# Kernel optimization log

Hardware: AMD Instinct MI355X
Metric: run time of the kernel (lower is better)

The kernel has to match this reference:

```python
import jax, jax.numpy as jnp
import numpy as np

B, N, I = 8, 1024, 64
E, H, D = 2, 2, 128   # edge types, heads per layer, hidden dim
O = 64                # num_outputs
IN1 = E * H * D       # layer-1 filter input dim (concat of layer-0 heads)


def setup_inputs() -> dict:
    key = jax.random.key(0)
    ks = jax.random.split(key, 20)
    s = lambda f: 1.0 / np.sqrt(f)
    inp = {
        "nodes": jax.random.normal(ks[0], (B, N, I), jnp.float32),
        "edges": jax.random.normal(ks[1], (B, N, N, E), jnp.float32) * 0.1,
        "Wemb": jax.random.normal(ks[2], (I, D), jnp.float32) * s(I),
        "bemb": jnp.zeros((D,), jnp.float32),
        # layer 0 params: filter W, att nets a1/a2 (weight + bias), state bias
        "W0":   jax.random.normal(ks[3], (E, H, D, D), jnp.float32) * s(D),
        "A1w0": jax.random.normal(ks[4], (E, H, D), jnp.float32) * s(D),
        "A1b0": jnp.zeros((E, H), jnp.float32),
        "A2w0": jax.random.normal(ks[5], (E, H, D), jnp.float32) * s(D),
        "A2b0": jnp.zeros((E, H), jnp.float32),
        "SB0":  jnp.zeros((E, H, D), jnp.float32),
        # layer 1 params (input dim = E*H*D from concat)
        "W1":   jax.random.normal(ks[6], (E, H, IN1, D), jnp.float32) * s(IN1),
        "A1w1": jax.random.normal(ks[7], (E, H, D), jnp.float32) * s(D),
        "A1b1": jnp.zeros((E, H), jnp.float32),
        "A2w1": jax.random.normal(ks[8], (E, H, D), jnp.float32) * s(D),
        "A2b1": jnp.zeros((E, H), jnp.float32),
        "SB1":  jnp.zeros((E, H, D), jnp.float32),
        "Wout": jax.random.normal(ks[9], (D, O), jnp.float32) * s(D),
        "bout": jnp.zeros((O,), jnp.float32),
    }
    return inp


def _gat_layer(state, edges_ebnn, W, a1w, a1b, a2w, a2b, sb):
    # state: (B,N,Fin); W: (E,H,Fin,D); edges_ebnn: (E,1,B,N,N)
    Wh = jnp.einsum('bni,ehid->ehbnd', state, W)                    # (E,H,B,N,D)
    s1 = jnp.einsum('ehbnd,ehd->ehbn', Wh, a1w) + a1b[:, :, None, None]
    s2 = jnp.einsum('ehbnd,ehd->ehbn', Wh, a2w) + a2b[:, :, None, None]
    att = s1[..., :, None] + s2[..., None, :]                       # a1_i + a2_j
    att = jax.nn.leaky_relu(att, 0.2) + edges_ebnn                  # edge-type bias
    att = jax.nn.softmax(att, axis=-2)                              # torch dim=1 (over i)
    msg = jnp.einsum('ehbij,ehbjd->ehbid', att, Wh)                 # bmm aggregation
    return msg + sb[:, :, None, None, :]                            # (E,H,B,N,D)


def reference(nodes, edges, Wemb, bemb,
              W0, A1w0, A1b0, A2w0, A2b0, SB0,
              W1, A1w1, A1b1, A2w1, A2b1, SB1,
              Wout, bout):
    edges_e = jnp.transpose(edges, (3, 0, 1, 2))[:, None]           # (E,1,B,N,N)
    state = jax.nn.relu(nodes @ Wemb + bemb)                        # SlimFC embedding
    # layer 0: concat heads/edgetypes along feature dim (torch order jj outer, ii inner)
    m0 = _gat_layer(state, edges_e, W0, A1w0, A1b0, A2w0, A2b0, SB0)
    state = jnp.transpose(m0, (2, 3, 0, 1, 4)).reshape(B, N, E * H * D)
    # layer 1 (last): elu then mean over all heads/edgetypes
    m1 = jax.nn.elu(_gat_layer(state, edges_e, W1, A1w1, A1b1, A2w1, A2b1, SB1))
    state = jnp.mean(m1, axis=(0, 1))                               # (B,N,D)
    return state @ Wout + bout                                      # (B,N,O)
```

## Files before the change

kernel.cpp:

```cpp
#include <hip/hip_runtime.h>
#include <math.h>

#define NB 8
#define NN 1024
#define NI 64
#define EHC 4
#define ND 128
#define NO 64
#define FIN1 512
#define BN 8192
#define LOG2E 1.4426950408889634f

typedef __attribute__((ext_vector_type(8))) short short8;
typedef __attribute__((ext_vector_type(4))) float f32x4;
typedef __attribute__((ext_vector_type(2))) unsigned uint32x2;

__device__ __forceinline__ unsigned short f2bf(float f) {
    union { float f; unsigned u; } v; v.f = f;
    unsigned r = v.u + 0x7FFF + ((v.u >> 16) & 1);
    return (unsigned short)(r >> 16);
}
__device__ __forceinline__ unsigned short f2h(float f) {
    union { _Float16 h; unsigned short u; } v;
    v.h = (_Float16)f;
    return v.u;
}
__device__ __forceinline__ float h2f(unsigned short u) {
    union { unsigned short u; _Float16 h; } v;
    v.u = u;
    return (float)v.h;
}

__global__ void prepTk(const float* __restrict__ W0, const float* __restrict__ W1,
                       const float* __restrict__ Wemb, unsigned short* __restrict__ W0T,
                       unsigned short* __restrict__ W1T, unsigned short* __restrict__ WembT) {
    int idx = blockIdx.x * 256 + threadIdx.x;
    if (idx < EHC * ND * ND) {
        int eh = idx >> 14, d = (idx >> 7) & 127, k = idx & 127;
        W0T[idx] = f2bf(W0[((size_t)(eh * ND + k)) * ND + d]);
    }
    int idx1 = idx - EHC * ND * ND;
    if (idx1 >= 0 && idx1 < EHC * ND * FIN1) {
        int eh = idx1 >> 16;
        int r = idx1 & 65535;
        int d = r >> 9, k = r & 511;
        W1T[idx1] = f2bf(W1[((size_t)(eh * FIN1 + k)) * ND + d]);
    }
    int idx2 = idx - (EHC * ND * ND + EHC * ND * FIN1);
    if (idx2 >= 0 && idx2 < ND * NI) {
        int d = idx2 >> 6, k = idx2 & 63;
        WembT[idx2] = f2bf(Wemb[k * ND + d]);
    }
}

__global__ __launch_bounds__(256, 4) void embwh0k(
    const float* __restrict__ nodes, const unsigned short* __restrict__ WembT,
    const float* __restrict__ bemb, const unsigned short* __restrict__ W0T,
    unsigned short* __restrict__ WhT, const float* __restrict__ a1w,
    const float* __restrict__ a1b, const float* __restrict__ a2w,
    const float* __restrict__ a2b, float* __restrict__ s1, float* __restrict__ s2) {
    int id = blockIdx.x;
    int g = id & 7, s_ = id >> 3;
    int eh = s_ & 3;
    int row0 = ((s_ >> 2) * 8 + g) * 32;
    int t = threadIdx.x;
    int w = t >> 6, lane = t & 63;
    int m = lane & 15, quad = lane >> 4;

    __shared__ unsigned short stateL[32 * 136];

    f32x4 accE[2][2];
#pragma unroll
    for (int mt = 0; mt < 2; ++mt)
#pragma unroll
        for (int nt = 0; nt < 2; ++nt) accE[mt][nt] = (f32x4){0.f, 0.f, 0.f, 0.f};
#pragma unroll
    for (int kt = 0; kt < 2; ++kt) {
        short8 aE[2], bE[2];
#pragma unroll
        for (int mt = 0; mt < 2; ++mt) {
            const float* np = nodes + (size_t)(row0 + mt * 16 + m) * NI + kt * 32 + quad * 8;
            f32x4 v0 = *(const f32x4*)np;
            f32x4 v1 = *(const f32x4*)(np + 4);
            union { unsigned short us[8]; short8 s8; } pk;
#pragma unroll
            for (int r = 0; r < 4; ++r) {
                pk.us[r] = f2bf(v0[r]);
                pk.us[r + 4] = f2bf(v1[r]);
            }
            aE[mt] = pk.s8;
        }
#pragma unroll
        for (int nt = 0; nt < 2; ++nt)
            bE[nt] = *(const short8*)(WembT + (w * 32 + nt * 16 + m) * NI + kt * 32 + quad * 8);
#pragma unroll
        for (int mt = 0; mt < 2; ++mt)
#pragma unroll
            for (int nt = 0; nt < 2; ++nt)
                accE[mt][nt] =
                    __builtin_amdgcn_mfma_f32_16x16x32_bf16(aE[mt], bE[nt], accE[mt][nt], 0, 0, 0);
    }
#pragma unroll
    for (int mt = 0; mt < 2; ++mt)
#pragma unroll
        for (int nt = 0; nt < 2; ++nt) {
            int d = w * 32 + nt * 16 + m;
            float bb = bemb[d];
#pragma unroll
            for (int r = 0; r < 4; ++r) {
                float v = fmaxf(accE[mt][nt][r] + bb, 0.f);
                stateL[(mt * 16 + quad * 4 + r) * 136 + d] = f2bf(v);
            }
        }
    __syncthreads();

    f32x4 acc[2][2];
#pragma unroll
    for (int mt = 0; mt < 2; ++mt)
#pragma unroll
        for (int nt = 0; nt < 2; ++nt) acc[mt][nt] = (f32x4){0.f, 0.f, 0.f, 0.f};
#pragma unroll
    for (int k0 = 0; k0 < ND; k0 += 32) {
        short8 a[2], b[2];
#pragma unroll
        for (int mt = 0; mt < 2; ++mt)
            a[mt] = *(const short8*)&stateL[(mt * 16 + m) * 136 + k0 + quad * 8];
#pragma unroll
        for (int nt = 0; nt < 2; ++nt)
            b[nt] = *(const short8*)(W0T + ((size_t)(eh * ND + w * 32 + nt * 16 + m)) * ND +
                                     k0 + quad * 8);
#pragma unroll
        for (int mt = 0; mt < 2; ++mt)
#pragma unroll
            for (int nt = 0; nt < 2; ++nt)
                acc[mt][nt] =
                    __builtin_amdgcn_mfma_f32_16x16x32_bf16(a[mt], b[nt], acc[mt][nt], 0, 0, 0);
    }

    int b_ = row0 >> 10, i0b = row0 & 1023;
    int ehb = eh * NB + b_;
#pragma unroll
    for (int mt = 0; mt < 2; ++mt)
#pragma unroll
        for (int nt = 0; nt < 2; ++nt) {
            int d = w * 32 + nt * 16 + m;
            int i = i0b + mt * 16 + quad * 4;
            union { unsigned short us[4]; unsigned long long u64; } pk;
#pragma unroll
            for (int r = 0; r < 4; ++r) pk.us[r] = f2bf(acc[mt][nt][r]);
            *(unsigned long long*)(WhT + (((size_t)ehb) * ND + d) * NN + i) = pk.u64;
        }
    float w1a = a1w[eh * ND + w * 32 + m], w1b = a1w[eh * ND + w * 32 + 16 + m];
    float w2a = a2w[eh * ND + w * 32 + m], w2b = a2w[eh * ND + w * 32 + 16 + m];
    float p1[2][4], p2[2][4];
#pragma unroll
    for (int mt = 0; mt < 2; ++mt)
#pragma unroll
        for (int r = 0; r < 4; ++r) {
            p1[mt][r] = acc[mt][0][r] * w1a + acc[mt][1][r] * w1b;
            p2[mt][r] = acc[mt][0][r] * w2a + acc[mt][1][r] * w2b;
        }
#pragma unroll
    for (int off = 8; off >= 1; off >>= 1)
#pragma unroll
        for (int mt = 0; mt < 2; ++mt)
#pragma unroll
            for (int r = 0; r < 4; ++r) {
                p1[mt][r] += __shfl_xor(p1[mt][r], off);
                p2[mt][r] += __shfl_xor(p2[mt][r], off);
            }
    __shared__ float sred[2][4][4][8];
    if (m == 0) {
#pragma unroll
        for (int mt = 0; mt < 2; ++mt)
#pragma unroll
            for (int r = 0; r < 4; ++r) {
                sred[0][w][quad][mt * 4 + r] = p1[mt][r];
                sred[1][w][quad][mt * 4 + r] = p2[mt][r];
            }
    }
    __syncthreads();
    if (t < 32) {
        int mt = t >> 4, quad2 = (t >> 2) & 3, r = t & 3;
        int c = mt * 4 + r;
        float v = sred[0][0][quad2][c] + sred[0][1][quad2][c] + sred[0][2][quad2][c] +
                  sred[0][3][quad2][c];
        s1[(size_t)ehb * NN + i0b + t] = (v + a1b[eh]) * LOG2E;
    } else if (t < 64) {
        int tl = t - 32;
        int mt = tl >> 4, quad2 = (tl >> 2) & 3, r = tl & 3;
        int c = mt * 4 + r;
        float v = sred[1][0][quad2][c] + sred[1][1][quad2][c] + sred[1][2][quad2][c] +
                  sred[1][3][quad2][c];
        s2[(size_t)ehb * NN + i0b + tl] = (v + a2b[eh]) * LOG2E;
    }
}

__global__ __launch_bounds__(256, 4) void whgemm1k(
    const unsigned short* __restrict__ state, const unsigned short* __restrict__ WT,
    unsigned short* __restrict__ WhT, const float* __restrict__ a1w,
    const float* __restrict__ a1b, const float* __restrict__ a2w,
    const float* __restrict__ a2b, float* __restrict__ s1, float* __restrict__ s2) {
    int id = blockIdx.x;
    int g = id & 7, s_ = id >> 3;
    int eh = s_ & 3;
    int row0 = ((s_ >> 2) * 8 + g) * 32;
    int t = threadIdx.x;
    int w = t >> 6, lane = t & 63;
    int m = lane & 15, quad = lane >> 4;

    f32x4 acc[2][2];
#pragma unroll
    for (int mt = 0; mt < 2; ++mt)
#pragma unroll
        for (int nt = 0; nt < 2; ++nt) acc[mt][nt] = (f32x4){0.f, 0.f, 0.f, 0.f};

    const unsigned short* Ab = state + (size_t)(row0 + m) * FIN1 + quad * 8;
    const unsigned short* Bb = WT + ((size_t)eh * ND + w * 32 + m) * FIN1 + quad * 8;
#pragma unroll 4
    for (int k0 = 0; k0 < FIN1; k0 += 32) {
        short8 a[2], b[2];
#pragma unroll
        for (int mt = 0; mt < 2; ++mt)
            a[mt] = *(const short8*)(Ab + (size_t)mt * 16 * FIN1 + k0);
#pragma unroll
        for (int nt = 0; nt < 2; ++nt)
            b[nt] = *(const short8*)(Bb + (size_t)nt * 16 * FIN1 + k0);
#pragma unroll
        for (int mt = 0; mt < 2; ++mt)
#pragma unroll
            for (int nt = 0; nt < 2; ++nt)
                acc[mt][nt] =
                    __builtin_amdgcn_mfma_f32_16x16x32_bf16(a[mt], b[nt], acc[mt][nt], 0, 0, 0);
    }
    int b_ = row0 >> 10, i0b = row0 & 1023;
    int ehb = eh * NB + b_;
#pragma unroll
    for (int mt = 0; mt < 2; ++mt)
#pragma unroll
        for (int nt = 0; nt < 2; ++nt) {
            int d = w * 32 + nt * 16 + m;
            int i = i0b + mt * 16 + quad * 4;
            union { unsigned short us[4]; unsigned long long u64; } pk;
#pragma unroll
            for (int r = 0; r < 4; ++r) pk.us[r] = f2bf(acc[mt][nt][r]);
            *(unsigned long long*)(WhT + (((size_t)ehb) * ND + d) * NN + i) = pk.u64;
        }
    float w1a = a1w[eh * ND + w * 32 + m], w1b = a1w[eh * ND + w * 32 + 16 + m];
    float w2a = a2w[eh * ND + w * 32 + m], w2b = a2w[eh * ND + w * 32 + 16 + m];
    float p1[2][4], p2[2][4];
#pragma unroll
    for (int mt = 0; mt < 2; ++mt)
#pragma unroll
        for (int r = 0; r < 4; ++r) {
            p1[mt][r] = acc[mt][0][r] * w1a + acc[mt][1][r] * w1b;
            p2[mt][r] = acc[mt][0][r] * w2a + acc[mt][1][r] * w2b;
        }
#pragma unroll
    for (int off = 8; off >= 1; off >>= 1)
#pragma unroll
        for (int mt = 0; mt < 2; ++mt)
#pragma unroll
            for (int r = 0; r < 4; ++r) {
                p1[mt][r] += __shfl_xor(p1[mt][r], off);
                p2[mt][r] += __shfl_xor(p2[mt][r], off);
            }
    __shared__ float sred[2][4][4][8];
    if (m == 0) {
#pragma unroll
        for (int mt = 0; mt < 2; ++mt)
#pragma unroll
            for (int r = 0; r < 4; ++r) {
                sred[0][w][quad][mt * 4 + r] = p1[mt][r];
                sred[1][w][quad][mt * 4 + r] = p2[mt][r];
            }
    }
    __syncthreads();
    if (t < 32) {
        int mt = t >> 4, quad2 = (t >> 2) & 3, r = t & 3;
        int c = mt * 4 + r;
        float v = sred[0][0][quad2][c] + sred[0][1][quad2][c] + sred[0][2][quad2][c] +
                  sred[0][3][quad2][c];
        s1[(size_t)ehb * NN + i0b + t] = (v + a1b[eh]) * LOG2E;
    } else if (t < 64) {
        int tl = t - 32;
        int mt = tl >> 4, quad2 = (tl >> 2) & 3, r = tl & 3;
        int c = mt * 4 + r;
        float v = sred[1][0][quad2][c] + sred[1][1][quad2][c] + sred[1][2][quad2][c] +
                  sred[1][3][quad2][c];
        s2[(size_t)ehb * NN + i0b + tl] = (v + a2b[eh]) * LOG2E;
    }
}

template <int CONV>
__global__ __launch_bounds__(256, 4) void colsumk(const float* __restrict__ edges,
                                                  unsigned* __restrict__ edgesH,
                                                  const float* __restrict__ s1,
                                                  const float* __restrict__ s2,
                                                  float* __restrict__ Spart) {
    int jt = blockIdx.x, b = blockIdx.y, ic = blockIdx.z;
    int t = threadIdx.x;
    int jp = t & 31, is = t >> 5;
    int j = jt * 64 + jp * 2;
    __shared__ float s1L[4][128];
    for (int idx = t; idx < 512; idx += 256) {
        int eh = idx >> 7;
        s1L[eh][idx & 127] = s1[((size_t)eh * NB + b) * NN + ic * 128 + (idx & 127)];
    }
    __syncthreads();
    float s2v[4][2], acc4[4][2];
#pragma unroll
    for (int eh = 0; eh < 4; ++eh) {
        s2v[eh][0] = s2[((size_t)eh * NB + b) * NN + j];
        s2v[eh][1] = s2[((size_t)eh * NB + b) * NN + j + 1];
        acc4[eh][0] = 0.f;
        acc4[eh][1] = 0.f;
    }
    int irow0 = ic * 128 + is * 16;
    const float4* ep = (const float4*)edges + (size_t)(b * NN + irow0) * (NN / 2) + jt * 32 + jp;
    unsigned* ehw = edgesH + (size_t)(b * NN + irow0) * NN + j;
#pragma unroll 4
    for (int ii = 0; ii < 16; ++ii) {
        float e00, e10, e01, e11;
        if (CONV) {
            float4 ev = ep[(size_t)ii * (NN / 2)];
            unsigned p0 = (unsigned)f2h(ev.x * LOG2E) | ((unsigned)f2h(ev.y * LOG2E) << 16);
            unsigned p1 = (unsigned)f2h(ev.z * LOG2E) | ((unsigned)f2h(ev.w * LOG2E) << 16);
            *(uint32x2*)(ehw + (size_t)ii * NN) = (uint32x2){p0, p1};
            e00 = h2f((unsigned short)(p0 & 0xffff));
            e10 = h2f((unsigned short)(p0 >> 16));
            e01 = h2f((unsigned short)(p1 & 0xffff));
            e11 = h2f((unsigned short)(p1 >> 16));
        } else {
            uint32x2 pk = *(const uint32x2*)(ehw + (size_t)ii * NN);
            e00 = h2f((unsigned short)(pk.x & 0xffff));
            e10 = h2f((unsigned short)(pk.x >> 16));
            e01 = h2f((unsigned short)(pk.y & 0xffff));
            e11 = h2f((unsigned short)(pk.y >> 16));
        }
#pragma unroll
        for (int eh = 0; eh < 4; ++eh) {
            float sv = s1L[eh][is * 16 + ii];
            float x0 = sv + s2v[eh][0];
            x0 = fmaxf(x0, 0.2f * x0);
            acc4[eh][0] += __builtin_exp2f(x0 + (eh < 2 ? e00 : e10));
            float x1 = sv + s2v[eh][1];
            x1 = fmaxf(x1, 0.2f * x1);
            acc4[eh][1] += __builtin_exp2f(x1 + (eh < 2 ? e01 : e11));
        }
    }
    __shared__ float red[8][4][64];
#pragma unroll
    for (int eh = 0; eh < 4; ++eh) {
        red[is][eh][jp * 2] = acc4[eh][0];
        red[is][eh][jp * 2 + 1] = acc4[eh][1];
    }
    __syncthreads();
    if (t < 256) {
        int eho = t >> 6, jlo = t & 63;
        float Sv = 0.f;
#pragma unroll
        for (int isx = 0; isx < 8; ++isx) Sv += red[isx][eho][jlo];
        Spart[(((size_t)ic * EHC + eho) * NB + b) * NN + jt * 64 + jlo] = Sv;
    }
}

__global__ __launch_bounds__(512, 4) void msgk(const unsigned* __restrict__ edgesH,
                                               const unsigned short* __restrict__ WhT,
                                               const float* __restrict__ s1,
                                               const float* __restrict__ s2,
                                               const float* __restrict__ Spart,
                                               const float* __restrict__ sb,
                                               unsigned short* __restrict__ out0,
                                               float* __restrict__ out1, int mode) {
    int id = blockIdx.x;
    int b = id & 7;
    int s_ = id >> 3;
    int eh = s_ & 3;
    int itile = s_ >> 2;
    int e = eh >> 1;
    int i0 = itile * 64;
    int t = threadIdx.x;
    int w = t >> 6, lane = t & 63;
    int n = lane & 15, quad = lane >> 4;
    int jl = t & 63, ib = w;

    __shared__ float2 stL[NN];
    __shared__ unsigned short pA[2][64 * 72];

    int base = (eh * NB + b) * NN;
    const size_t pstr = (size_t)EHC * NB * NN;
    for (int jj = t; jj < NN; jj += 512) {
        float S = 0.f;
#pragma unroll
        for (int ic = 0; ic < 8; ++ic) S += Spart[(size_t)ic * pstr + base + jj];
        stL[jj] = make_float2(s2[base + jj], __builtin_log2f(S));
    }
    float s1r[8];
    {
        const f32x4* sp = (const f32x4*)(s1 + base + i0 + ib * 8);
        f32x4 v0 = sp[0], v1 = sp[1];
#pragma unroll
        for (int r = 0; r < 4; ++r) { s1r[r] = v0[r]; s1r[r + 4] = v1[r]; }
    }

    f32x4 acc[4];
#pragma unroll
    for (int nt = 0; nt < 4; ++nt) acc[nt] = (f32x4){0.f, 0.f, 0.f, 0.f};

    const unsigned short* Ab =
        WhT + ((size_t)base * ND + (size_t)(w * 16 + n) * NN) + quad * 8;
    const unsigned* ep = edgesH + (size_t)(b * NN + i0 + ib * 8) * NN + jl;
    __syncthreads();

    unsigned evA[8], evB[8];
    short8 aA[2], aB[2];

    auto loadE = [&](unsigned* ev, int j0) {
#pragma unroll
        for (int q = 0; q < 8; ++q) ev[q] = ep[(size_t)q * NN + j0];
    };
    auto loadA = [&](short8* av, int j0) {
#pragma unroll
        for (int kt = 0; kt < 2; ++kt)
            av[kt] = *(const short8*)(Ab + kt * 32 + j0);
    };
    auto pstep = [&](const unsigned* ev, const short8* av, int j0, int buf) {
        float2 stj = stL[j0 + jl];
#pragma unroll
        for (int q = 0; q < 8; ++q) {
            float edge = h2f((unsigned short)(e ? (ev[q] >> 16) : (ev[q] & 0xffff)));
            float x = s1r[q] + stj.x;
            x = fmaxf(x, 0.2f * x);
            pA[buf][(ib * 8 + q) * 72 + jl] = f2bf(__builtin_exp2f(x + edge - stj.y));
        }
        __syncthreads();
#pragma unroll
        for (int kt = 0; kt < 2; ++kt) {
            short8 bv[4];
#pragma unroll
            for (int nt = 0; nt < 4; ++nt)
                bv[nt] = *(const short8*)&pA[buf][(nt * 16 + n) * 72 + kt * 32 + quad * 8];
#pragma unroll
            for (int nt = 0; nt < 4; ++nt)
                acc[nt] =
                    __builtin_amdgcn_mfma_f32_16x16x32_bf16(av[kt], bv[nt], acc[nt], 0, 0, 0);
        }
    };

    loadE(evA, 0);
    loadA(aA, 0);
    for (int sp2 = 0; sp2 < 8; ++sp2) {
        int j0 = sp2 * 128;
        loadE(evB, j0 + 64);
        loadA(aB, j0 + 64);
        pstep(evA, aA, j0, 0);
        if (sp2 < 7) {
            loadE(evA, j0 + 128);
            loadA(aA, j0 + 128);
        }
        pstep(evB, aB, j0 + 64, 1);
    }

    {
        int d0 = w * 16 + quad * 4;
        f32x4 sbv = *(const f32x4*)&sb[eh * ND + d0];
#pragma unroll
        for (int nt = 0; nt < 4; ++nt) {
            int i = i0 + nt * 16 + n;
            if (mode == 0) {
                union { unsigned short us[4]; unsigned long long u64; } pk;
#pragma unroll
                for (int r = 0; r < 4; ++r) pk.us[r] = f2bf(acc[nt][r] + sbv[r]);
                *(unsigned long long*)(out0 + (size_t)(b * NN + i) * FIN1 + eh * ND + d0) =
                    pk.u64;
            } else {
                f32x4 vv;
#pragma unroll
                for (int r = 0; r < 4; ++r) {
                    float v = acc[nt][r] + sbv[r];
                    vv[r] = v > 0.f ? v : expm1f(v);
                }
                *(f32x4*)(out1 + ((size_t)(eh * NB + b) * NN + i) * ND + d0) = vv;
            }
        }
    }
}

__global__ __launch_bounds__(256) void finalk(const float* __restrict__ m1,
                                              const float* __restrict__ Wout,
                                              const float* __restrict__ bout,
                                              float* __restrict__ out) {
    int row0 = blockIdx.x * 16;
    int t = threadIdx.x;
    __shared__ float sF[16 * ND];
    __shared__ float wL[ND * NO];
    const size_t str = (size_t)BN * ND;
    for (int idx = t; idx < 16 * ND; idx += 256) {
        size_t r = (size_t)row0 * ND + idx;
        sF[idx] = 0.25f * (m1[r] + m1[r + str] + m1[r + 2 * str] + m1[r + 3 * str]);
    }
    for (int idx = t; idx < ND * NO; idx += 256) wL[idx] = Wout[idx];
    __syncthreads();
    int o = t & 63;
    int rr = t >> 6;
    float bo = bout[o];
#pragma unroll
    for (int q = 0; q < 4; ++q) {
        int r = rr * 4 + q;
        float acc = 0.f;
#pragma unroll 4
        for (int d = 0; d < ND; ++d) acc += sF[r * ND + d] * wL[d * NO + o];
        out[(size_t)(row0 + r) * NO + o] = acc + bo;
    }
}

extern "C" void kernel_launch(void* const* d_in, const int* in_sizes, int n_in,
                              void* d_out, int out_size, void* d_ws, size_t ws_size,
                              hipStream_t stream) {
    const float* nodes = (const float*)d_in[0];
    const float* edges = (const float*)d_in[1];
    const float* Wemb = (const float*)d_in[2];
    const float* bemb = (const float*)d_in[3];
    const float* W0 = (const float*)d_in[4];
    const float* A1w0 = (const float*)d_in[5];
    const float* A1b0 = (const float*)d_in[6];
    const float* A2w0 = (const float*)d_in[7];
    const float* A2b0 = (const float*)d_in[8];
    const float* SB0 = (const float*)d_in[9];
    const float* W1 = (const float*)d_in[10];
    const float* A1w1 = (const float*)d_in[11];
    const float* A1b1 = (const float*)d_in[12];
    const float* A2w1 = (const float*)d_in[13];
    const float* A2b1 = (const float*)d_in[14];
    const float* SB1 = (const float*)d_in[15];
    const float* Wout = (const float*)d_in[16];
    const float* bout = (const float*)d_in[17];
    float* out = (float*)d_out;

    char* p = (char*)d_ws;
    auto alloc = [&](size_t bytes) {
        char* r = p;
        p += (bytes + 255) & ~(size_t)255;
        return r;
    };
    unsigned short* W0T = (unsigned short*)alloc((size_t)EHC * ND * ND * 2);
    unsigned short* W1T = (unsigned short*)alloc((size_t)EHC * ND * FIN1 * 2);
    unsigned short* WembT = (unsigned short*)alloc((size_t)ND * NI * 2);
    unsigned short* WhT = (unsigned short*)alloc((size_t)EHC * BN * ND * 2);
    unsigned short* state1 = (unsigned short*)alloc((size_t)BN * FIN1 * 2);
    float* s1b = (float*)alloc((size_t)EHC * BN * 4);
    float* s2b = (float*)alloc((size_t)EHC * BN * 4);
    float* Spart = (float*)alloc((size_t)8 * EHC * BN * 4);
    float* m1 = (float*)alloc((size_t)EHC * BN * ND * 4);
    unsigned* edgesH = (unsigned*)alloc((size_t)NB * NN * NN * 4);

    prepTk<<<1312, 256, 0, stream>>>(W0, W1, Wemb, W0T, W1T, WembT);
    embwh0k<<<1024, 256, 0, stream>>>(nodes, WembT, bemb, W0T, WhT, A1w0, A1b0, A2w0, A2b0,
                                      s1b, s2b);
    colsumk<1><<<dim3(NN / 64, NB, 8), 256, 0, stream>>>(edges, edgesH, s1b, s2b, Spart);
    msgk<<<512, 512, 0, stream>>>(edgesH, WhT, s1b, s2b, Spart, SB0, state1, m1, 0);
    whgemm1k<<<1024, 256, 0, stream>>>(state1, W1T, WhT, A1w1, A1b1, A2w1, A2b1, s1b, s2b);
    colsumk<0><<<dim3(NN / 64, NB, 8), 256, 0, stream>>>(edges, edgesH, s1b, s2b, Spart);
    msgk<<<512, 512, 0, stream>>>(edgesH, WhT, s1b, s2b, Spart, SB1, state1, m1, 1);
    finalk<<<BN / 16, 256, 0, stream>>>(m1, Wout, bout, out);
}
```

Measured before the change: 267.4 us.

## Fuse ELU, head mean and output projection into msgk; halve i-tile

The final projection kernel is removed. The layer-1 message kernel now applies ELU, stages the result as bf16 in LDS, multiplies it by a transposed bf16 Wout with MFMA, and atomically accumulates a quarter of each head's contribution into the zeroed output buffer, which whgemm1k clears. The i-tile is halved to 32 rows so twice as many blocks launch, with a higher occupancy target. This drops the fp32 m1 round-trip through memory and one launch, but adds float atomics (order-dependent summation), bf16 rounding before the projection, and a doubled count of column-sum reloads per block.

```diff
diff --git a/kernel.cpp b/kernel.cpp
--- a/kernel.cpp
+++ b/kernel.cpp
@@ -32,8 +32,9 @@
 }
 
 __global__ void prepTk(const float* __restrict__ W0, const float* __restrict__ W1,
-                       const float* __restrict__ Wemb, unsigned short* __restrict__ W0T,
-                       unsigned short* __restrict__ W1T, unsigned short* __restrict__ WembT) {
+                       const float* __restrict__ Wemb, const float* __restrict__ Wout,
+                       unsigned short* __restrict__ W0T, unsigned short* __restrict__ W1T,
+                       unsigned short* __restrict__ WembT, unsigned short* __restrict__ WoutT) {
     int idx = blockIdx.x * 256 + threadIdx.x;
     if (idx < EHC * ND * ND) {
         int eh = idx >> 14, d = (idx >> 7) & 127, k = idx & 127;
@@ -50,6 +51,11 @@
     if (idx2 >= 0 && idx2 < ND * NI) {
         int d = idx2 >> 6, k = idx2 & 63;
         WembT[idx2] = f2bf(Wemb[k * ND + d]);
+    }
+    int idx3 = idx - (EHC * ND * ND + EHC * ND * FIN1 + ND * NI);
+    if (idx3 >= 0 && idx3 < ND * NO) {
+        int o = idx3 >> 7, d = idx3 & 127;
+        WoutT[idx3] = f2bf(Wout[d * NO + o]);
     }
 }
 
@@ -200,7 +206,8 @@
     const unsigned short* __restrict__ state, const unsigned short* __restrict__ WT,
     unsigned short* __restrict__ WhT, const float* __restrict__ a1w,
     const float* __restrict__ a1b, const float* __restrict__ a2w,
-    const float* __restrict__ a2b, float* __restrict__ s1, float* __restrict__ s2) {
+    const float* __restrict__ a2b, float* __restrict__ s1, float* __restrict__ s2,
+    float* __restrict__ outz) {
     int id = blockIdx.x;
     int g = id & 7, s_ = id >> 3;
     int eh = s_ & 3;
@@ -208,6 +215,11 @@
     int t = threadIdx.x;
     int w = t >> 6, lane = t & 63;
     int m = lane & 15, quad = lane >> 4;
+
+    {
+        f32x4 z = (f32x4){0.f, 0.f, 0.f, 0.f};
+        for (int idx = t; idx < 128; idx += 256) ((f32x4*)outz)[(size_t)id * 128 + idx] = z;
+    }
 
     f32x4 acc[2][2];
 #pragma unroll
@@ -365,28 +377,30 @@
     }
 }
 
-__global__ __launch_bounds__(512, 4) void msgk(const unsigned* __restrict__ edgesH,
+__global__ __launch_bounds__(512, 8) void msgk(const unsigned* __restrict__ edgesH,
                                                const unsigned short* __restrict__ WhT,
                                                const float* __restrict__ s1,
                                                const float* __restrict__ s2,
                                                const float* __restrict__ Spart,
                                                const float* __restrict__ sb,
                                                unsigned short* __restrict__ out0,
-                                               float* __restrict__ out1, int mode) {
+                                               const unsigned short* __restrict__ WoutT,
+                                               const float* __restrict__ bout,
+                                               float* __restrict__ out, int mode) {
     int id = blockIdx.x;
     int b = id & 7;
     int s_ = id >> 3;
     int eh = s_ & 3;
     int itile = s_ >> 2;
     int e = eh >> 1;
-    int i0 = itile * 64;
+    int i0 = itile * 32;
     int t = threadIdx.x;
     int w = t >> 6, lane = t & 63;
     int n = lane & 15, quad = lane >> 4;
     int jl = t & 63, ib = w;
 
     __shared__ float2 stL[NN];
-    __shared__ unsigned short pA[2][64 * 72];
+    __shared__ unsigned short pA[2][32 * 72];
 
     int base = (eh * NB + b) * NN;
     const size_t pstr = (size_t)EHC * NB * NN;
@@ -396,29 +410,28 @@
         for (int ic = 0; ic < 8; ++ic) S += Spart[(size_t)ic * pstr + base + jj];
         stL[jj] = make_float2(s2[base + jj], __builtin_log2f(S));
     }
-    float s1r[8];
+    float s1r[4];
     {
-        const f32x4* sp = (const f32x4*)(s1 + base + i0 + ib * 8);
-        f32x4 v0 = sp[0], v1 = sp[1];
-#pragma unroll
-        for (int r = 0; r < 4; ++r) { s1r[r] = v0[r]; s1r[r + 4] = v1[r]; }
-    }
-
-    f32x4 acc[4];
-#pragma unroll
-    for (int nt = 0; nt < 4; ++nt) acc[nt] = (f32x4){0.f, 0.f, 0.f, 0.f};
+        f32x4 v0 = *(const f32x4*)(s1 + base + i0 + ib * 4);
+#pragma unroll
+        for (int r = 0; r < 4; ++r) s1r[r] = v0[r];
+    }
+
+    f32x4 acc[2];
+#pragma unroll
+    for (int nt = 0; nt < 2; ++nt) acc[nt] = (f32x4){0.f, 0.f, 0.f, 0.f};
 
     const unsigned short* Ab =
         WhT + ((size_t)base * ND + (size_t)(w * 16 + n) * NN) + quad * 8;
-    const unsigned* ep = edgesH + (size_t)(b * NN + i0 + ib * 8) * NN + jl;
+    const unsigned* ep = edgesH + (size_t)(b * NN + i0 + ib * 4) * NN + jl;
     __syncthreads();
 
-    unsigned evA[8], evB[8];
+    unsigned evA[4], evB[4];
     short8 aA[2], aB[2];
 
     auto loadE = [&](unsigned* ev, int j0) {
 #pragma unroll
-        for (int q = 0; q < 8; ++q) ev[q] = ep[(size_t)q * NN + j0];
+        for (int q = 0; q < 4; ++q) ev[q] = ep[(size_t)q * NN + j0];
     };
     auto loadA = [&](short8* av, int j0) {
 #pragma unroll
@@ -428,21 +441,21 @@
     auto pstep = [&](const unsigned* ev, const short8* av, int j0, int buf) {
         float2 stj = stL[j0 + jl];
 #pragma unroll
-        for (int q = 0; q < 8; ++q) {
+        for (int q = 0; q < 4; ++q) {
             float edge = h2f((unsigned short)(e ? (ev[q] >> 16) : (ev[q] & 0xffff)));
             float x = s1r[q] + stj.x;
             x = fmaxf(x, 0.2f * x);
-            pA[buf][(ib * 8 + q) * 72 + jl] = f2bf(__builtin_exp2f(x + edge - stj.y));
+            pA[buf][(ib * 4 + q) * 72 + jl] = f2bf(__builtin_exp2f(x + edge - stj.y));
         }
         __syncthreads();
 #pragma unroll
         for (int kt = 0; kt < 2; ++kt) {
-            short8 bv[4];
-#pragma unroll
-            for (int nt = 0; nt < 4; ++nt)
+            short8 bv[2];
+#pragma unroll
+            for (int nt = 0; nt < 2; ++nt)
                 bv[nt] = *(const short8*)&pA[buf][(nt * 16 + n) * 72 + kt * 32 + quad * 8];
 #pragma unroll
-            for (int nt = 0; nt < 4; ++nt)
+            for (int nt = 0; nt < 2; ++nt)
                 acc[nt] =
                     __builtin_amdgcn_mfma_f32_16x16x32_bf16(av[kt], bv[nt], acc[nt], 0, 0, 0);
         }
@@ -462,56 +475,45 @@
         pstep(evB, aB, j0 + 64, 1);
     }
 
-    {
-        int d0 = w * 16 + quad * 4;
-        f32x4 sbv = *(const f32x4*)&sb[eh * ND + d0];
-#pragma unroll
-        for (int nt = 0; nt < 4; ++nt) {
+    int d0 = w * 16 + quad * 4;
+    f32x4 sbv = *(const f32x4*)&sb[eh * ND + d0];
+    if (mode == 0) {
+#pragma unroll
+        for (int nt = 0; nt < 2; ++nt) {
             int i = i0 + nt * 16 + n;
-            if (mode == 0) {
-                union { unsigned short us[4]; unsigned long long u64; } pk;
-#pragma unroll
-                for (int r = 0; r < 4; ++r) pk.us[r] = f2bf(acc[nt][r] + sbv[r]);
-                *(unsigned long long*)(out0 + (size_t)(b * NN + i) * FIN1 + eh * ND + d0) =
-                    pk.u64;
-            } else {
-                f32x4 vv;
-#pragma unroll
-                for (int r = 0; r < 4; ++r) {
-                    float v = acc[nt][r] + sbv[r];
-                    vv[r] = v > 0.f ? v : expm1f(v);
-                }
-                *(f32x4*)(out1 + ((size_t)(eh * NB + b) * NN + i) * ND + d0) = vv;
-            }
-        }
-    }
-}
-
-__global__ __launch_bounds__(256) void finalk(const float* __restrict__ m1,
-                                              const float* __restrict__ Wout,
-                                              const float* __restrict__ bout,
-                                              float* __restrict__ out) {
-    int row0 = blockIdx.x * 16;
-    int t = threadIdx.x;
-    __shared__ float sF[16 * ND];
-    __shared__ float wL[ND * NO];
-    const size_t str = (size_t)BN * ND;
-    for (int idx = t; idx < 16 * ND; idx += 256) {
-        size_t r = (size_t)row0 * ND + idx;
-        sF[idx] = 0.25f * (m1[r] + m1[r + str] + m1[r + 2 * str] + m1[r + 3 * str]);
-    }
-    for (int idx = t; idx < ND * NO; idx += 256) wL[idx] = Wout[idx];
-    __syncthreads();
-    int o = t & 63;
-    int rr = t >> 6;
-    float bo = bout[o];
-#pragma unroll
-    for (int q = 0; q < 4; ++q) {
-        int r = rr * 4 + q;
-        float acc = 0.f;
-#pragma unroll 4
-        for (int d = 0; d < ND; ++d) acc += sF[r * ND + d] * wL[d * NO + o];
-        out[(size_t)(row0 + r) * NO + o] = acc + bo;
+            union { unsigned short us[4]; unsigned long long u64; } pk;
+#pragma unroll
+            for (int r = 0; r < 4; ++r) pk.us[r] = f2bf(acc[nt][r] + sbv[r]);
+            *(unsigned long long*)(out0 + (size_t)(b * NN + i) * FIN1 + eh * ND + d0) = pk.u64;
+        }
+    } else {
+        __syncthreads();
+        unsigned short* eluL = (unsigned short*)pA;
+#pragma unroll
+        for (int nt = 0; nt < 2; ++nt) {
+            int il = nt * 16 + n;
+#pragma unroll
+            for (int r = 0; r < 4; ++r) {
+                float v = acc[nt][r] + sbv[r];
+                v = v > 0.f ? v : expm1f(v);
+                eluL[il * 136 + d0 + r] = f2bf(v);
+            }
+        }
+        __syncthreads();
+        int it = w & 1, ot = w >> 1;
+        f32x4 hacc = (f32x4){0.f, 0.f, 0.f, 0.f};
+#pragma unroll
+        for (int k0 = 0; k0 < ND; k0 += 32) {
+            short8 av = *(const short8*)&eluL[(it * 16 + n) * 136 + k0 + quad * 8];
+            short8 bv = *(const short8*)(WoutT + (ot * 16 + n) * ND + k0 + quad * 8);
+            hacc = __builtin_amdgcn_mfma_f32_16x16x32_bf16(av, bv, hacc, 0, 0, 0);
+        }
+        int o = ot * 16 + n;
+        float bo = bout[o];
+        float* op = out + (size_t)(b * NN + i0 + it * 16 + quad * 4) * NO + o;
+#pragma unroll
+        for (int r = 0; r < 4; ++r)
+            atomicAdd(op + (size_t)r * NO, 0.25f * hacc[r] + 0.25f * bo);
     }
 }
 
@@ -547,21 +549,23 @@
     unsigned short* W0T = (unsigned short*)alloc((size_t)EHC * ND * ND * 2);
     unsigned short* W1T = (unsigned short*)alloc((size_t)EHC * ND * FIN1 * 2);
     unsigned short* WembT = (unsigned short*)alloc((size_t)ND * NI * 2);
+    unsigned short* WoutT = (unsigned short*)alloc((size_t)ND * NO * 2);
     unsigned short* WhT = (unsigned short*)alloc((size_t)EHC * BN * ND * 2);
     unsigned short* state1 = (unsigned short*)alloc((size_t)BN * FIN1 * 2);
     float* s1b = (float*)alloc((size_t)EHC * BN * 4);
     float* s2b = (float*)alloc((size_t)EHC * BN * 4);
     float* Spart = (float*)alloc((size_t)8 * EHC * BN * 4);
-    float* m1 = (float*)alloc((size_t)EHC * BN * ND * 4);
     unsigned* edgesH = (unsigned*)alloc((size_t)NB * NN * NN * 4);
 
-    prepTk<<<1312, 256, 0, stream>>>(W0, W1, Wemb, W0T, W1T, WembT);
+    prepTk<<<1344, 256, 0, stream>>>(W0, W1, Wemb, Wout, W0T, W1T, WembT, WoutT);
     embwh0k<<<1024, 256, 0, stream>>>(nodes, WembT, bemb, W0T, WhT, A1w0, A1b0, A2w0, A2b0,
                                       s1b, s2b);
     colsumk<1><<<dim3(NN / 64, NB, 8), 256, 0, stream>>>(edges, edgesH, s1b, s2b, Spart);
-    msgk<<<512, 512, 0, stream>>>(edgesH, WhT, s1b, s2b, Spart, SB0, state1, m1, 0);
-    whgemm1k<<<1024, 256, 0, stream>>>(state1, W1T, WhT, A1w1, A1b1, A2w1, A2b1, s1b, s2b);
+    msgk<<<1024, 512, 0, stream>>>(edgesH, WhT, s1b, s2b, Spart, SB0, state1, WoutT, bout,
+                                   out, 0);
+    whgemm1k<<<1024, 256, 0, stream>>>(state1, W1T, WhT, A1w1, A1b1, A2w1, A2b1, s1b, s2b,
+                                       out);
     colsumk<0><<<dim3(NN / 64, NB, 8), 256, 0, stream>>>(edges, edgesH, s1b, s2b, Spart);
-    msgk<<<512, 512, 0, stream>>>(edgesH, WhT, s1b, s2b, Spart, SB1, state1, m1, 1);
-    finalk<<<BN / 16, 256, 0, stream>>>(m1, Wout, bout, out);
-}
+    msgk<<<1024, 512, 0, stream>>>(edgesH, WhT, s1b, s2b, Spart, SB1, state1, WoutT, bout,
+                                   out, 1);
+}
```

New measurement: 281.4 us. 1.05x slower.
